# Kernel optimization log

Hardware: AMD Instinct MI355X
Metric: run time of the kernel (lower is better)

## Reference

```python
import jax, jax.numpy as jnp
import numpy as np

D_MODEL = 1024
H = 16
D_K = D_MODEL // H  # 64


def setup_inputs() -> dict:
    key = jax.random.key(0)
    ks = jax.random.split(key, 10)
    B, S = 4, 4096
    q = jax.random.normal(ks[0], (B, S, D_MODEL), dtype=jnp.float32)
    k = jax.random.normal(ks[1], (B, S, D_MODEL), dtype=jnp.float32)
    v = jax.random.normal(ks[2], (B, S, D_MODEL), dtype=jnp.float32)
    m = jax.random.uniform(ks[3], (B, S), dtype=jnp.float32)
    sc = 1.0 / np.sqrt(D_MODEL)
    Wq = jax.random.uniform(ks[4], (D_MODEL, D_K), jnp.float32, -sc, sc)
    bq = jax.random.uniform(ks[5], (D_K,), jnp.float32, -sc, sc)
    Wk = jax.random.uniform(ks[6], (D_MODEL, D_K), jnp.float32, -sc, sc)
    bk = jax.random.uniform(ks[7], (D_K,), jnp.float32, -sc, sc)
    Wv = jax.random.uniform(ks[8], (D_MODEL, D_K), jnp.float32, -sc, sc)
    bv = jax.random.uniform(ks[9], (D_K,), jnp.float32, -sc, sc)
    return {"q": q, "k": k, "v": v, "m": m,
            "Wq": Wq, "bq": bq, "Wk": Wk, "bk": bk, "Wv": Wv, "bv": bv}


def reference(q, k, v, m, Wq, bq, Wk, bk, Wv, bv):
    # single-head projections: [B,S,d_model] -> [B,S,d_k]
    qh = q @ Wq + bq
    kh = k @ Wk + bk
    vh = v @ Wv + bv
    # scaled dot-product scores [B,S,S]
    a = jnp.einsum("bqd,bkd->bqk", qh, kh) / jnp.sqrt(jnp.float32(D_K))
    # multiplicative per-query-row mask BEFORE softmax (non-standard variant)
    a = a * m[:, :, None]
    a = jax.nn.softmax(a, axis=-1)
    # AV: [B,S,S] x [B,S,d_k] -> [B,S,d_k]
    y = jnp.einsum("bqk,bkd->bqd", a, vh)
    return y
```

## Files before the change

### kernel.cpp

```cpp
#include <hip/hip_runtime.h>


typedef __attribute__((ext_vector_type(8))) short short8;
typedef __attribute__((ext_vector_type(4))) float float4v;
typedef __attribute__((ext_vector_type(4))) unsigned int uint4v;

#define DEV static __device__ __forceinline__

DEV unsigned short f2bf(float f) {
  unsigned int x; __builtin_memcpy(&x, &f, 4);
  x += 0x7fff + ((x >> 16) & 1);
  return (unsigned short)(x >> 16);
}

__global__ __launch_bounds__(256) void transpose_w(
    const float* __restrict__ Wq, const float* __restrict__ Wk,
    const float* __restrict__ Wv, unsigned short* __restrict__ WT) {
  int idx = blockIdx.x * 256 + threadIdx.x;
  int p = idx >> 16;
  int r = idx & 65535;
  int kk = r >> 6, d = r & 63;
  const float* W = (p == 0) ? Wq : (p == 1) ? Wk : Wv;
  WT[p * 65536 + d * 1024 + kk] = f2bf(W[r]);
}

__global__ __launch_bounds__(256, 6) void proj_kernel(
    const float* __restrict__ xq, const float* __restrict__ xk,
    const float* __restrict__ xv, const float* __restrict__ mmask,
    const float* __restrict__ bq, const float* __restrict__ bk,
    const float* __restrict__ bv, const unsigned short* __restrict__ WT,
    unsigned short* __restrict__ qs, unsigned short* __restrict__ khh,
    unsigned short* __restrict__ vhT) {
  constexpr int LDSTR = 136;
  __shared__ __align__(16) unsigned short Xs[32 * LDSTR];
  __shared__ __align__(16) unsigned short Ws[64 * LDSTR];

  const int p = blockIdx.x >> 9;
  const int rt = blockIdx.x & 511;
  const int row0 = rt * 32;
  const int t = threadIdx.x;
  const int w = t >> 6, ln = t & 63;
  const int lr = ln & 15, quad = ln >> 4;

  const float* X = (p == 0) ? xq : (p == 1) ? xk : xv;
  const unsigned short* WTp = WT + p * 65536;
  const float* Xbase = X + (size_t)row0 * 1024;

  float4v acc[2];
#pragma unroll
  for (int i = 0; i < 2; ++i) acc[i] = (float4v){0.f, 0.f, 0.f, 0.f};

  const int xr_row = t >> 5, xr_col = (t & 31) * 4;
  const int wr_row = t >> 4, wr_col = (t & 15) * 8;
  const float* Xsrc = Xbase + (size_t)xr_row * 1024 + xr_col;
  const unsigned short* Wsrc = WTp + (size_t)wr_row * 1024 + wr_col;
  unsigned short* Xdst = &Xs[xr_row * LDSTR + xr_col];
  unsigned short* Wdst = &Ws[wr_row * LDSTR + wr_col];

  float4v xr[4];
  uint4v wr[4];

#define ISSUE(kc_)                                                         \
  {                                                                        \
    const int k0_ = (kc_) * 128;                                           \
    _Pragma("unroll") for (int i = 0; i < 4; ++i) {                        \
      xr[i] = *(const float4v*)(Xsrc + (size_t)i * 8 * 1024 + k0_);        \
      wr[i] = *(const uint4v*)(Wsrc + (size_t)i * 16 * 1024 + k0_);        \
    }                                                                      \
  }

  ISSUE(0);
  for (int kc = 0; kc < 8; ++kc) {
#pragma unroll
    for (int i = 0; i < 4; ++i) {
      unsigned short tmp[4];
#pragma unroll
      for (int j = 0; j < 4; ++j) tmp[j] = f2bf(xr[i][j]);
      __builtin_memcpy(Xdst + i * 8 * LDSTR, tmp, 8);
    }
#pragma unroll
    for (int i = 0; i < 4; ++i)
      *(uint4v*)(Wdst + i * 16 * LDSTR) = wr[i];
    __syncthreads();
    if (kc < 7) ISSUE(kc + 1);

    if (p < 2) {
      const int rb = w & 1, cb = w >> 1;
#pragma unroll
      for (int ks = 0; ks < 4; ++ks) {
        short8 af = *(const short8*)&Xs[(rb * 16 + lr) * LDSTR + ks * 32 + quad * 8];
#pragma unroll
        for (int ct = 0; ct < 2; ++ct) {
          short8 bf = *(const short8*)&Ws[(cb * 32 + ct * 16 + lr) * LDSTR + ks * 32 + quad * 8];
          acc[ct] = __builtin_amdgcn_mfma_f32_16x16x32_bf16(af, bf, acc[ct], 0, 0, 0);
        }
      }
    } else {
#pragma unroll
      for (int ks = 0; ks < 4; ++ks) {
        short8 af = *(const short8*)&Ws[(w * 16 + lr) * LDSTR + ks * 32 + quad * 8];
#pragma unroll
        for (int ct = 0; ct < 2; ++ct) {
          short8 bf = *(const short8*)&Xs[(ct * 16 + lr) * LDSTR + ks * 32 + quad * 8];
          acc[ct] = __builtin_amdgcn_mfma_f32_16x16x32_bf16(af, bf, acc[ct], 0, 0, 0);
        }
      }
    }
    __syncthreads();
  }
#undef ISSUE

  if (p == 0) {
    const float L2E8 = 1.4426950408889634f * 0.125f;
    const int rb = w & 1, cb = w >> 1;
#pragma unroll
    for (int r = 0; r < 4; ++r) {
      int sg = row0 + rb * 16 + quad * 4 + r;
      float mv = mmask[sg] * L2E8;
#pragma unroll
      for (int ct = 0; ct < 2; ++ct) {
        int d = cb * 32 + ct * 16 + lr;
        qs[(size_t)sg * 64 + d] = f2bf((acc[ct][r] + bq[d]) * mv);
      }
    }
  } else if (p == 1) {
    const int rb = w & 1, cb = w >> 1;
#pragma unroll
    for (int r = 0; r < 4; ++r) {
      int sg = row0 + rb * 16 + quad * 4 + r;
#pragma unroll
      for (int ct = 0; ct < 2; ++ct) {
        int d = cb * 32 + ct * 16 + lr;
        khh[(size_t)sg * 64 + d] = f2bf(acc[ct][r] + bk[d]);
      }
    }
  } else {
    int b = row0 >> 12, sloc = row0 & 4095;
#pragma unroll
    for (int r = 0; r < 4; ++r) {
      int d = w * 16 + quad * 4 + r;
      float bias = bv[d];
#pragma unroll
      for (int ct = 0; ct < 2; ++ct) {
        int sg = sloc + ct * 16 + lr;
        vhT[(size_t)b * 64 * 4096 + (size_t)d * 4096 + sg] = f2bf(acc[ct][r] + bias);
      }
    }
  }
}

#define SPLITS 4
__global__ __launch_bounds__(256) void attn_split(
    const unsigned short* __restrict__ qs, const unsigned short* __restrict__ khh,
    const unsigned short* __restrict__ vhT, float* __restrict__ O_part,
    float* __restrict__ L_part) {
  constexpr int LDSTR = 88;
  __shared__ __align__(16) unsigned short Ks[64 * LDSTR];
  __shared__ __align__(16) unsigned short Vs[64 * LDSTR];
  __shared__ __align__(16) unsigned short Ps[4 * 16 * LDSTR];

  const int split = blockIdx.x >> 8;
  const int rest  = blockIdx.x & 255;
  const int b = rest >> 6;
  const int s0 = (rest & 63) * 64;
  const int t = threadIdx.x, w = t >> 6, ln = t & 63;
  const int lr = ln & 15, quad = ln >> 4;

  const size_t qrow = (size_t)(b * 4096 + s0 + w * 16 + lr) * 64;
  short8 qf0 = *(const short8*)&qs[qrow + quad * 8];
  short8 qf1 = *(const short8*)&qs[qrow + 32 + quad * 8];

  float Lacc[4] = {0.f, 0.f, 0.f, 0.f};
  float4v O[4];
#pragma unroll
  for (int i = 0; i < 4; ++i) O[i] = (float4v){0.f, 0.f, 0.f, 0.f};

  const int srow = t >> 3, scol = (t & 7) * 8;
  const unsigned short* Kg = khh + (size_t)b * 4096 * 64;
  const unsigned short* Vg = vhT + (size_t)b * 64 * 4096;
  unsigned short* Pw = Ps + w * 16 * LDSTR;

  uint4v kr[2], vr[2];

#define ISSUE_KV(kt_)                                                       \
  {                                                                         \
    const int k0_ = split * 1024 + (kt_) * 64;                              \
    _Pragma("unroll") for (int ps = 0; ps < 2; ++ps) {                      \
      const int rr = srow + ps * 32;                                        \
      kr[ps] = *(const uint4v*)&Kg[(size_t)(k0_ + rr) * 64 + scol];         \
      vr[ps] = *(const uint4v*)&Vg[(size_t)rr * 4096 + k0_ + scol];         \
    }                                                                       \
  }

  ISSUE_KV(0);
  for (int kt = 0; kt < 16; ++kt) {
#pragma unroll
    for (int ps = 0; ps < 2; ++ps) {
      const int rr = srow + ps * 32;
      *(uint4v*)&Ks[rr * LDSTR + scol] = kr[ps];
      *(uint4v*)&Vs[rr * LDSTR + scol] = vr[ps];
    }
    __syncthreads();
    if (kt < 15) ISSUE_KV(kt + 1);

    float4v sc[4];
#pragma unroll
    for (int ct = 0; ct < 4; ++ct) {
      sc[ct] = (float4v){0.f, 0.f, 0.f, 0.f};
      short8 kf0 = *(const short8*)&Ks[(ct * 16 + lr) * LDSTR + quad * 8];
      short8 kf1 = *(const short8*)&Ks[(ct * 16 + lr) * LDSTR + 32 + quad * 8];
      sc[ct] = __builtin_amdgcn_mfma_f32_16x16x32_bf16(qf0, kf0, sc[ct], 0, 0, 0);
      sc[ct] = __builtin_amdgcn_mfma_f32_16x16x32_bf16(qf1, kf1, sc[ct], 0, 0, 0);
    }

#pragma unroll
    for (int ct = 0; ct < 4; ++ct)
#pragma unroll
      for (int r = 0; r < 4; ++r) {
        float pv = exp2f(sc[ct][r]);
        Lacc[r] += pv;
        Pw[(quad * 4 + r) * LDSTR + ct * 16 + lr] = f2bf(pv);
      }

    __asm__ volatile("s_waitcnt lgkmcnt(0)" ::: "memory");

    short8 pf0 = *(const short8*)&Pw[lr * LDSTR + quad * 8];
    short8 pf1 = *(const short8*)&Pw[lr * LDSTR + 32 + quad * 8];
#pragma unroll
    for (int dt = 0; dt < 4; ++dt) {
      short8 vf0 = *(const short8*)&Vs[(dt * 16 + lr) * LDSTR + quad * 8];
      short8 vf1 = *(const short8*)&Vs[(dt * 16 + lr) * LDSTR + 32 + quad * 8];
      O[dt] = __builtin_amdgcn_mfma_f32_16x16x32_bf16(pf0, vf0, O[dt], 0, 0, 0);
      O[dt] = __builtin_amdgcn_mfma_f32_16x16x32_bf16(pf1, vf1, O[dt], 0, 0, 0);
    }
    __syncthreads();
  }
#undef ISSUE_KV

#pragma unroll
  for (int r = 0; r < 4; ++r) {
    float s = Lacc[r];
    s += __shfl_xor(s, 1);
    s += __shfl_xor(s, 2);
    s += __shfl_xor(s, 4);
    s += __shfl_xor(s, 8);
    Lacc[r] = s;
  }

#pragma unroll
  for (int r = 0; r < 4; ++r) {
    int prow = b * 4096 + s0 + w * 16 + quad * 4 + r;
    size_t obase = ((size_t)split * 16384 + prow) * 64;
#pragma unroll
    for (int dt = 0; dt < 4; ++dt)
      O_part[obase + dt * 16 + lr] = O[dt][r];
    if (lr == 0) L_part[(size_t)split * 16384 + prow] = Lacc[r];
  }
}

__global__ __launch_bounds__(256) void attn_reduce(
    const float* __restrict__ O_part, const float* __restrict__ L_part,
    float* __restrict__ out) {
  size_t idx = (size_t)blockIdx.x * 256 + threadIdx.x;
  size_t row = idx >> 6;
  float l = L_part[row] + L_part[16384 + row] + L_part[2 * 16384 + row] +
            L_part[3 * 16384 + row];
  float o = O_part[idx] + O_part[idx + (size_t)16384 * 64] +
            O_part[idx + (size_t)2 * 16384 * 64] +
            O_part[idx + (size_t)3 * 16384 * 64];
  out[idx] = o / l;
}

extern "C" void kernel_launch(void* const* d_in, const int* in_sizes, int n_in,
                              void* d_out, int out_size, void* d_ws, size_t ws_size,
                              hipStream_t stream) {
  const float* q  = (const float*)d_in[0];
  const float* k  = (const float*)d_in[1];
  const float* v  = (const float*)d_in[2];
  const float* m  = (const float*)d_in[3];
  const float* Wq = (const float*)d_in[4];
  const float* bq = (const float*)d_in[5];
  const float* Wk = (const float*)d_in[6];
  const float* bk = (const float*)d_in[7];
  const float* Wv = (const float*)d_in[8];
  const float* bv = (const float*)d_in[9];
  float* out = (float*)d_out;

  unsigned short* ws16 = (unsigned short*)d_ws;
  unsigned short* WT  = ws16;
  unsigned short* qs  = WT + 3 * 65536;
  unsigned short* kh  = qs + 16384 * 64;
  unsigned short* vhT = kh + 16384 * 64;
  float* O_part = (float*)(vhT + 16384 * 64);
  float* L_part = O_part + (size_t)SPLITS * 16384 * 64;

  transpose_w<<<dim3(768), dim3(256), 0, stream>>>(Wq, Wk, Wv, WT);
  proj_kernel<<<dim3(1536), dim3(256), 0, stream>>>(q, k, v, m, bq, bk, bv, WT,
                                                    qs, kh, vhT);
  attn_split<<<dim3(SPLITS * 256), dim3(256), 0, stream>>>(qs, kh, vhT,
                                                           O_part, L_part);
  attn_reduce<<<dim3(4096), dim3(256), 0, stream>>>(O_part, L_part, out);
}
```

Baseline: 263.7 us.

## Load K/V MFMA fragments directly from global memory and vectorize split reduction

```diff
diff --git a/kernel.cpp b/kernel.cpp
--- a/kernel.cpp
+++ b/kernel.cpp
@@ -65,7 +65,7 @@
     const int k0_ = (kc_) * 128;                                           \
     _Pragma("unroll") for (int i = 0; i < 4; ++i) {                        \
       xr[i] = *(const float4v*)(Xsrc + (size_t)i * 8 * 1024 + k0_);        \
-      wr[i] = *(const uint4v*)(Wsrc + (size_t)i * 16 * 1024 + k0_);        \
+      wr[i] = *(const uint4v*)(Wsrc + (size_t)i * 16 * 1024 + k0_);       \
     }                                                                      \
   }
 
@@ -155,8 +155,6 @@
     const unsigned short* __restrict__ vhT, float* __restrict__ O_part,
     float* __restrict__ L_part) {
   constexpr int LDSTR = 88;
-  __shared__ __align__(16) unsigned short Ks[64 * LDSTR];
-  __shared__ __align__(16) unsigned short Vs[64 * LDSTR];
   __shared__ __align__(16) unsigned short Ps[4 * 16 * LDSTR];
 
   const int split = blockIdx.x >> 8;
@@ -175,40 +173,20 @@
 #pragma unroll
   for (int i = 0; i < 4; ++i) O[i] = (float4v){0.f, 0.f, 0.f, 0.f};
 
-  const int srow = t >> 3, scol = (t & 7) * 8;
   const unsigned short* Kg = khh + (size_t)b * 4096 * 64;
   const unsigned short* Vg = vhT + (size_t)b * 64 * 4096;
   unsigned short* Pw = Ps + w * 16 * LDSTR;
 
-  uint4v kr[2], vr[2];
-
-#define ISSUE_KV(kt_)                                                       \
-  {                                                                         \
-    const int k0_ = split * 1024 + (kt_) * 64;                              \
-    _Pragma("unroll") for (int ps = 0; ps < 2; ++ps) {                      \
-      const int rr = srow + ps * 32;                                        \
-      kr[ps] = *(const uint4v*)&Kg[(size_t)(k0_ + rr) * 64 + scol];         \
-      vr[ps] = *(const uint4v*)&Vg[(size_t)rr * 4096 + k0_ + scol];         \
-    }                                                                       \
-  }
-
-  ISSUE_KV(0);
   for (int kt = 0; kt < 16; ++kt) {
-#pragma unroll
-    for (int ps = 0; ps < 2; ++ps) {
-      const int rr = srow + ps * 32;
-      *(uint4v*)&Ks[rr * LDSTR + scol] = kr[ps];
-      *(uint4v*)&Vs[rr * LDSTR + scol] = vr[ps];
-    }
-    __syncthreads();
-    if (kt < 15) ISSUE_KV(kt + 1);
+    const int k0 = split * 1024 + kt * 64;
 
     float4v sc[4];
 #pragma unroll
     for (int ct = 0; ct < 4; ++ct) {
+      const unsigned short* kb = Kg + (size_t)(k0 + ct * 16 + lr) * 64 + quad * 8;
+      short8 kf0 = *(const short8*)kb;
+      short8 kf1 = *(const short8*)(kb + 32);
       sc[ct] = (float4v){0.f, 0.f, 0.f, 0.f};
-      short8 kf0 = *(const short8*)&Ks[(ct * 16 + lr) * LDSTR + quad * 8];
-      short8 kf1 = *(const short8*)&Ks[(ct * 16 + lr) * LDSTR + 32 + quad * 8];
       sc[ct] = __builtin_amdgcn_mfma_f32_16x16x32_bf16(qf0, kf0, sc[ct], 0, 0, 0);
       sc[ct] = __builtin_amdgcn_mfma_f32_16x16x32_bf16(qf1, kf1, sc[ct], 0, 0, 0);
     }
@@ -228,14 +206,13 @@
     short8 pf1 = *(const short8*)&Pw[lr * LDSTR + 32 + quad * 8];
 #pragma unroll
     for (int dt = 0; dt < 4; ++dt) {
-      short8 vf0 = *(const short8*)&Vs[(dt * 16 + lr) * LDSTR + quad * 8];
-      short8 vf1 = *(const short8*)&Vs[(dt * 16 + lr) * LDSTR + 32 + quad * 8];
+      const unsigned short* vb = Vg + (size_t)(dt * 16 + lr) * 4096 + k0 + quad * 8;
+      short8 vf0 = *(const short8*)vb;
+      short8 vf1 = *(const short8*)(vb + 32);
       O[dt] = __builtin_amdgcn_mfma_f32_16x16x32_bf16(pf0, vf0, O[dt], 0, 0, 0);
       O[dt] = __builtin_amdgcn_mfma_f32_16x16x32_bf16(pf1, vf1, O[dt], 0, 0, 0);
     }
-    __syncthreads();
-  }
-#undef ISSUE_KV
+  }
 
 #pragma unroll
   for (int r = 0; r < 4; ++r) {
@@ -261,14 +238,21 @@
 __global__ __launch_bounds__(256) void attn_reduce(
     const float* __restrict__ O_part, const float* __restrict__ L_part,
     float* __restrict__ out) {
-  size_t idx = (size_t)blockIdx.x * 256 + threadIdx.x;
-  size_t row = idx >> 6;
+  size_t i4 = (size_t)blockIdx.x * 256 + threadIdx.x;
+  size_t row = i4 >> 4;
   float l = L_part[row] + L_part[16384 + row] + L_part[2 * 16384 + row] +
             L_part[3 * 16384 + row];
-  float o = O_part[idx] + O_part[idx + (size_t)16384 * 64] +
-            O_part[idx + (size_t)2 * 16384 * 64] +
-            O_part[idx + (size_t)3 * 16384 * 64];
-  out[idx] = o / l;
+  const size_t STRIDE = (size_t)16384 * 64 / 4;
+  const float4v* OP = (const float4v*)O_part;
+  float4v o = OP[i4];
+  float4v o1 = OP[i4 + STRIDE];
+  float4v o2 = OP[i4 + 2 * STRIDE];
+  float4v o3 = OP[i4 + 3 * STRIDE];
+  float inv = 1.0f / l;
+  float4v r;
+#pragma unroll
+  for (int j = 0; j < 4; ++j) r[j] = (o[j] + o1[j] + o2[j] + o3[j]) * inv;
+  ((float4v*)out)[i4] = r;
 }
 
 extern "C" void kernel_launch(void* const* d_in, const int* in_sizes, int n_in,
@@ -299,5 +283,5 @@
                                                     qs, kh, vhT);
   attn_split<<<dim3(SPLITS * 256), dim3(256), 0, stream>>>(qs, kh, vhT,
                                                            O_part, L_part);
-  attn_reduce<<<dim3(4096), dim3(256), 0, stream>>>(O_part, L_part, out);
-}
+  attn_reduce<<<dim3(1024), dim3(256), 0, stream>>>(O_part, L_part, out);
+}
```

Result: slower. 339.6 us (+28.8%).
